# Kernel tuning notes

Hardware: AMD Instinct MI355X
Metric: run time of the kernel (lower is better)

The kernel has to match this reference:

```python
import jax, jax.numpy as jnp
import numpy as np

DIM = 512        # token feature dim
HID = 1024       # expert hidden dim (dim * 2)
E = 16           # num_experts
N = 8192         # num tokens
TOPK = 2         # experts active per token (routing sparsity)


def setup_inputs() -> dict:
    key = jax.random.key(0)
    k_x, k_s, k_w1, k_w2 = jax.random.split(key, 4)
    x = jax.random.normal(k_x, (N, DIM), dtype=jnp.float32)
    # sparse routing scores: top-2 experts per token get nonzero score, rest 0
    scores = jax.random.uniform(k_s, (N, E), dtype=jnp.float32)
    vals, idx = jax.lax.top_k(scores, TOPK)
    routing_tensor = jnp.zeros((N, E), jnp.float32).at[jnp.arange(N)[:, None], idx].set(vals)
    # per-expert MLP params (depth=2, bias=True): Linear(DIM->HID), GELU, Linear(HID->DIM)
    W1 = jax.random.normal(k_w1, (E, DIM, HID), dtype=jnp.float32) * (1.0 / np.sqrt(DIM))
    b1 = jnp.zeros((E, HID), jnp.float32)
    W2 = jax.random.normal(k_w2, (E, HID, DIM), dtype=jnp.float32) * (1.0 / np.sqrt(HID))
    b2 = jnp.zeros((E, DIM), jnp.float32)
    return {"x": x, "routing_tensor": routing_tensor, "W1": W1, "b1": b1, "W2": W2, "b2": b2}


def reference(x, routing_tensor, W1, b1, W2, b2):
    # out[n] = sum_e routing[n,e] * MLP_e(x[n]); rows with score 0 contribute 0,
    # which is exactly the original mask-gather / scatter-add semantics.
    h = jax.nn.gelu(jnp.einsum('nd,edh->enh', x, W1) + b1[:, None, :], approximate=False)
    y = jnp.einsum('enh,ehd->end', h, W2) + b2[:, None, :]  # [E, N, DIM]
    return jnp.einsum('end,ne->nd', y, routing_tensor)       # combine weighted by scores
```

## Files before the change

### kernel.cpp

```cpp
#include <hip/hip_runtime.h>
#include <hip/hip_bf16.h>

#define NTOK 8192
#define DIM 512
#define HID 1024
#define NE 16
#define CAP 1280
#define MT 20

typedef __attribute__((ext_vector_type(8))) short short8;
typedef __attribute__((ext_vector_type(8))) unsigned short us8;
typedef __attribute__((ext_vector_type(4))) float f32x4;

static __device__ __forceinline__ unsigned short f2bf(float f) {
    __hip_bfloat16 h = __float2bfloat16(f);
    return __builtin_bit_cast(unsigned short, h);
}

static __device__ __forceinline__ void gl_lds16(const unsigned short* g, unsigned short* l) {
    __builtin_amdgcn_global_load_lds(
        (const __attribute__((address_space(1))) unsigned int*)g,
        (__attribute__((address_space(3))) unsigned int*)l, 16, 0, 0);
}

static __device__ __forceinline__ float gelu_f(float v) {
    float u = v * (0.7978845608f + 0.0356774081f * v * v);
    return v / (1.0f + __expf(-2.0f * u));
}

__global__ __launch_bounds__(256) void route_fill(const float* __restrict__ routing,
                                                  int* __restrict__ cnt,
                                                  int* __restrict__ sidx,
                                                  float* __restrict__ wtb) {
    __shared__ int lcnt[NE], lbase[NE];
    int t = threadIdx.x;
    int n = blockIdx.x * 256 + t;
    if (t < NE) lcnt[t] = 0;
    __syncthreads();
    int mye[2]; float myw[2]; int mypos[2]; int slot = 0;
    #pragma unroll
    for (int e = 0; e < NE; e++) {
        float r = routing[n * NE + e];
        if (r != 0.0f && slot < 2) {
            mye[slot] = e; myw[slot] = r;
            mypos[slot] = atomicAdd(&lcnt[e], 1);
            slot++;
        }
    }
    __syncthreads();
    if (t < NE) lbase[t] = atomicAdd(&cnt[t], lcnt[t]);
    __syncthreads();
    for (int s = 0; s < slot; s++) {
        int e = mye[s];
        int p = lbase[e] + mypos[s];
        if (p < CAP) { sidx[e * CAP + p] = n * 2 + s; wtb[e * CAP + p] = myw[s]; }
    }
}

__global__ __launch_bounds__(256) void prep2(const float* __restrict__ W1,
                                             const float* __restrict__ W2,
                                             unsigned short* __restrict__ w1t,
                                             unsigned short* __restrict__ w2t,
                                             const float* __restrict__ x,
                                             const int* __restrict__ cnt,
                                             const int* __restrict__ sidx,
                                             unsigned short* __restrict__ xg) {
    int b = blockIdx.x;
    int t = threadIdx.x;
    if (b < 4096) {
        __shared__ float tile[64][65];
        const float* src; unsigned short* dst; int R, C, bx, by;
        if (b < 2048) {
            int e = b >> 7, rem = b & 127; bx = rem & 15; by = rem >> 4;
            R = DIM; C = HID;
            src = W1 + (size_t)e * R * C; dst = w1t + (size_t)e * R * C;
        } else {
            int bb = b - 2048;
            int e = bb >> 7, rem = bb & 127; bx = rem & 7; by = rem >> 3;
            R = HID; C = DIM;
            src = W2 + (size_t)e * R * C; dst = w2t + (size_t)e * R * C;
        }
        int c0 = bx * 64, r0 = by * 64;
        int tx = t & 15, ty = t >> 4;
        #pragma unroll
        for (int i = 0; i < 4; i++) {
            float4 v = *(const float4*)(src + (size_t)(r0 + ty + i * 16) * C + c0 + tx * 4);
            tile[ty + i * 16][tx * 4 + 0] = v.x;
            tile[ty + i * 16][tx * 4 + 1] = v.y;
            tile[ty + i * 16][tx * 4 + 2] = v.z;
            tile[ty + i * 16][tx * 4 + 3] = v.w;
        }
        __syncthreads();
        int seg = t & 7;
        #pragma unroll
        for (int i = 0; i < 2; i++) {
            int dr = (t >> 3) + i * 32;
            us8 o;
            #pragma unroll
            for (int j = 0; j < 8; j++)
                o[j] = f2bf(tile[seg * 8 + j][dr]);
            *(us8*)(dst + (size_t)(c0 + dr) * R + r0 + seg * 8) = o;
        }
    } else {
        int gi = b - 4096;
        int lane = t & 63, rl = t >> 6;
        int row = gi * 4 + rl;
        int e = row / CAP, r = row - e * CAP;
        int c = cnt[e]; c = c > CAP ? CAP : c;
        us8 o;
        if (r < c) {
            int n = sidx[row] >> 1;
            const float* xr = x + (size_t)n * DIM + lane * 8;
            float4 v0 = *(const float4*)xr;
            float4 v1 = *(const float4*)(xr + 4);
            o[0] = f2bf(v0.x); o[1] = f2bf(v0.y); o[2] = f2bf(v0.z); o[3] = f2bf(v0.w);
            o[4] = f2bf(v1.x); o[5] = f2bf(v1.y); o[6] = f2bf(v1.z); o[7] = f2bf(v1.w);
        } else {
            #pragma unroll
            for (int j = 0; j < 8; j++) o[j] = 0;
        }
        *(us8*)(xg + (size_t)row * DIM + lane * 8) = o;
    }
}

template <int K>
__device__ __forceinline__ void mfma_main64(const unsigned short* __restrict__ A,
                                            const unsigned short* __restrict__ B,
                                            unsigned short* As, unsigned short* Bs,
                                            f32x4 acc[2][4]) {
    int t = threadIdx.x;
    int wave = t >> 6, lane = t & 63;
    int wm = wave >> 1, wn = wave & 1;
    int quad = lane >> 4, l16 = lane & 15;
    int lr = lane >> 3;
    int col = (lane & 7) << 3;
    for (int kc = 0; kc < K; kc += 64) {
        __syncthreads();
        #pragma unroll
        for (int j = 0; j < 2; j++) {
            int rb = wave * 16 + j * 8;
            gl_lds16(A + (size_t)(rb + lr) * K + kc + col, As + rb * 64);
        }
        #pragma unroll
        for (int j = 0; j < 4; j++) {
            int rb = wave * 32 + j * 8;
            gl_lds16(B + (size_t)(rb + lr) * K + kc + col, Bs + rb * 64);
        }
        __syncthreads();
        #pragma unroll
        for (int kk = 0; kk < 64; kk += 32) {
            short8 av[2], bv[4];
            #pragma unroll
            for (int mt = 0; mt < 2; mt++)
                av[mt] = *(const short8*)(&As[(wm * 32 + mt * 16 + l16) * 64 + kk + quad * 8]);
            #pragma unroll
            for (int nt = 0; nt < 4; nt++)
                bv[nt] = *(const short8*)(&Bs[(wn * 64 + nt * 16 + l16) * 64 + kk + quad * 8]);
            #pragma unroll
            for (int mt = 0; mt < 2; mt++)
                #pragma unroll
                for (int nt = 0; nt < 4; nt++)
                    acc[mt][nt] = __builtin_amdgcn_mfma_f32_16x16x32_bf16(
                        av[mt], bv[nt], acc[mt][nt], 0, 0, 0);
        }
    }
}


__global__ __launch_bounds__(256, 5) void gemm1_gelu(
    const unsigned short* __restrict__ xg, const unsigned short* __restrict__ w1t,
    const float* __restrict__ b1, const int* __restrict__ cnt,
    unsigned short* __restrict__ hbuf) {
    __shared__ __align__(16) unsigned short As[64 * 64];
    __shared__ __align__(16) unsigned short Bs[128 * 64];
    int L = blockIdx.x;
    int cc = L & 7, n = (L >> 3) & 7, g = L >> 6;
    int pi = cc + (g << 3);
    int e = pi / MT, m = pi % MT;
    int c = cnt[e]; c = c > CAP ? CAP : c;
    int m0 = m * 64;
    if (m0 >= c) return;
    int n0 = n * 128;
    const unsigned short* A = xg + ((size_t)e * CAP + m0) * DIM;
    const unsigned short* B = w1t + ((size_t)e * HID + n0) * DIM;
    f32x4 z = {0.f, 0.f, 0.f, 0.f};
    f32x4 acc[2][4];
    #pragma unroll
    for (int mt = 0; mt < 2; mt++)
        #pragma unroll
        for (int nt = 0; nt < 4; nt++) acc[mt][nt] = z;
    mfma_main64<DIM>(A, B, As, Bs, acc);
    int t = threadIdx.x;
    int wave = t >> 6, lane = t & 63;
    int wm = wave >> 1, wn = wave & 1, quad = lane >> 4, l16 = lane & 15;
    #pragma unroll
    for (int nt = 0; nt < 4; nt++) {
        int gn = n0 + wn * 64 + nt * 16 + l16;
        float bias = b1[e * HID + gn];
        #pragma unroll
        for (int mt = 0; mt < 2; mt++) {
            #pragma unroll
            for (int r = 0; r < 4; r++) {
                int gm = m0 + wm * 32 + mt * 16 + quad * 4 + r;
                float v = acc[mt][nt][r] + bias;
                hbuf[((size_t)e * CAP + gm) * HID + gn] = f2bf(gelu_f(v));
            }
        }
    }
}

__global__ __launch_bounds__(256, 5) void gemm2_store(
    const unsigned short* __restrict__ hbuf, const unsigned short* __restrict__ w2t,
    const float* __restrict__ b2, const int* __restrict__ cnt,
    const int* __restrict__ sidx, const float* __restrict__ wtb,
    float* __restrict__ ybuf) {
    __shared__ __align__(16) unsigned short As[64 * 64];
    __shared__ __align__(16) unsigned short Bs[128 * 64];
    int L = blockIdx.x;
    int cc = L & 7, n = (L >> 3) & 3, g = L >> 5;
    int pi = cc + (g << 3);
    int e = pi / MT, m = pi % MT;
    int c = cnt[e]; c = c > CAP ? CAP : c;
    int m0 = m * 64;
    if (m0 >= c) return;
    int n0 = n * 128;
    const unsigned short* A = hbuf + ((size_t)e * CAP + m0) * HID;
    const unsigned short* B = w2t + ((size_t)e * DIM + n0) * HID;
    f32x4 z = {0.f, 0.f, 0.f, 0.f};
    f32x4 acc[2][4];
    #pragma unroll
    for (int mt = 0; mt < 2; mt++)
        #pragma unroll
        for (int nt = 0; nt < 4; nt++) acc[mt][nt] = z;
    mfma_main64<HID>(A, B, As, Bs, acc);
    int t = threadIdx.x;
    int wave = t >> 6, lane = t & 63;
    int wm = wave >> 1, wn = wave & 1, quad = lane >> 4, l16 = lane & 15;
    #pragma unroll
    for (int mt = 0; mt < 2; mt++) {
        #pragma unroll
        for (int r = 0; r < 4; r++) {
            int gm = m0 + wm * 32 + mt * 16 + quad * 4 + r;
            if (gm < c) {
                int si = sidx[e * CAP + gm];
                float wgt = wtb[e * CAP + gm];
                float* yrow = ybuf + (size_t)si * DIM;
                #pragma unroll
                for (int nt = 0; nt < 4; nt++) {
                    int gn = n0 + wn * 64 + nt * 16 + l16;
                    yrow[gn] = wgt * (acc[mt][nt][r] + b2[e * DIM + gn]);
                }
            }
        }
    }
}

__global__ void combine(const float* __restrict__ yb, float* __restrict__ out) {
    int i = blockIdx.x * 256 + threadIdx.x;
    int n = i >> 7, d4 = i & 127;
    float4 a = ((const float4*)(yb + (size_t)(2 * n) * DIM))[d4];
    float4 b = ((const float4*)(yb + (size_t)(2 * n + 1) * DIM))[d4];
    float4 o;
    o.x = a.x + b.x; o.y = a.y + b.y; o.z = a.z + b.z; o.w = a.w + b.w;
    ((float4*)(out + (size_t)n * DIM))[d4] = o;
}

extern "C" void kernel_launch(void* const* d_in, const int* in_sizes, int n_in,
                              void* d_out, int out_size, void* d_ws, size_t ws_size,
                              hipStream_t stream) {
    const float* x       = (const float*)d_in[0];
    const float* routing = (const float*)d_in[1];
    const float* W1      = (const float*)d_in[2];
    const float* b1      = (const float*)d_in[3];
    const float* W2      = (const float*)d_in[4];
    const float* b2      = (const float*)d_in[5];
    float* out = (float*)d_out;

    char* w = (char*)d_ws;
    int*   cnt  = (int*)w;
    int*   sidx = (int*)(w + 256);
    float* wtb  = (float*)(w + 256 + NE * CAP * 4);
    char* base = w + 256 + NE * CAP * 8;
    unsigned short* xg  = (unsigned short*)base;
    unsigned short* hb  = xg + (size_t)NE * CAP * DIM;
    unsigned short* w1t = hb + (size_t)NE * CAP * HID;
    unsigned short* w2t = w1t + (size_t)NE * HID * DIM;
    float* ybuf = (float*)(w2t + (size_t)NE * DIM * HID);

    hipMemsetAsync(cnt, 0, 256, stream);

    route_fill<<<NTOK / 256, 256, 0, stream>>>(routing, cnt, sidx, wtb);
    prep2<<<4096 + 5120, 256, 0, stream>>>(W1, W2, w1t, w2t, x, cnt, sidx, xg);

    gemm1_gelu<<<8 * MT * NE, 256, 0, stream>>>(xg, w1t, b1, cnt, hb);
    gemm2_store<<<4 * MT * NE, 256, 0, stream>>>(hb, w2t, b2, cnt, sidx, wtb, ybuf);
    combine<<<(NTOK * DIM / 4) / 256, 256, 0, stream>>>(ybuf, out);
}
```

Before: 223.0 us.

## Store per-expert outputs in bf16 and hoist bias loads in gemm2

The intermediate per-(token,slot) output buffer changes from fp32 to bf16, which halves the scattered writes in gemm2 and the reads in the combine kernel. The combine kernel now processes 8 elements per thread, and gemm2 loads the b2 bias once per thread instead of inside the store loop. Launch bounds for both GEMMs rise from 5 to 6 waves per SIMD. In exchange, the output picks up extra bf16 rounding before the final fp32 sum, and the tighter launch bound may force register spills.

```diff
diff --git a/kernel.cpp b/kernel.cpp
--- a/kernel.cpp
+++ b/kernel.cpp
@@ -15,6 +15,10 @@
 static __device__ __forceinline__ unsigned short f2bf(float f) {
     __hip_bfloat16 h = __float2bfloat16(f);
     return __builtin_bit_cast(unsigned short, h);
+}
+static __device__ __forceinline__ float bf2f(unsigned short u) {
+    unsigned int v = (unsigned int)u << 16;
+    return __builtin_bit_cast(float, v);
 }
 
 static __device__ __forceinline__ void gl_lds16(const unsigned short* g, unsigned short* l) {
@@ -167,7 +171,7 @@
 }
 
 
-__global__ __launch_bounds__(256, 5) void gemm1_gelu(
+__global__ __launch_bounds__(256, 6) void gemm1_gelu(
     const unsigned short* __restrict__ xg, const unsigned short* __restrict__ w1t,
     const float* __restrict__ b1, const int* __restrict__ cnt,
     unsigned short* __restrict__ hbuf) {
@@ -209,11 +213,11 @@
     }
 }
 
-__global__ __launch_bounds__(256, 5) void gemm2_store(
+__global__ __launch_bounds__(256, 6) void gemm2_store(
     const unsigned short* __restrict__ hbuf, const unsigned short* __restrict__ w2t,
     const float* __restrict__ b2, const int* __restrict__ cnt,
     const int* __restrict__ sidx, const float* __restrict__ wtb,
-    float* __restrict__ ybuf) {
+    unsigned short* __restrict__ ybuf) {
     __shared__ __align__(16) unsigned short As[64 * 64];
     __shared__ __align__(16) unsigned short Bs[128 * 64];
     int L = blockIdx.x;
@@ -236,6 +240,10 @@
     int t = threadIdx.x;
     int wave = t >> 6, lane = t & 63;
     int wm = wave >> 1, wn = wave & 1, quad = lane >> 4, l16 = lane & 15;
+    float b2v[4];
+    #pragma unroll
+    for (int nt = 0; nt < 4; nt++)
+        b2v[nt] = b2[e * DIM + n0 + wn * 64 + nt * 16 + l16];
     #pragma unroll
     for (int mt = 0; mt < 2; mt++) {
         #pragma unroll
@@ -244,25 +252,30 @@
             if (gm < c) {
                 int si = sidx[e * CAP + gm];
                 float wgt = wtb[e * CAP + gm];
-                float* yrow = ybuf + (size_t)si * DIM;
+                unsigned short* yrow = ybuf + (size_t)si * DIM;
                 #pragma unroll
                 for (int nt = 0; nt < 4; nt++) {
                     int gn = n0 + wn * 64 + nt * 16 + l16;
-                    yrow[gn] = wgt * (acc[mt][nt][r] + b2[e * DIM + gn]);
+                    yrow[gn] = f2bf(wgt * (acc[mt][nt][r] + b2v[nt]));
                 }
             }
         }
     }
 }
 
-__global__ void combine(const float* __restrict__ yb, float* __restrict__ out) {
+__global__ void combine(const unsigned short* __restrict__ yb, float* __restrict__ out) {
     int i = blockIdx.x * 256 + threadIdx.x;
-    int n = i >> 7, d4 = i & 127;
-    float4 a = ((const float4*)(yb + (size_t)(2 * n) * DIM))[d4];
-    float4 b = ((const float4*)(yb + (size_t)(2 * n + 1) * DIM))[d4];
-    float4 o;
-    o.x = a.x + b.x; o.y = a.y + b.y; o.z = a.z + b.z; o.w = a.w + b.w;
-    ((float4*)(out + (size_t)n * DIM))[d4] = o;
+    int n = i >> 6, d8 = i & 63;
+    us8 a = ((const us8*)(yb + (size_t)(2 * n) * DIM))[d8];
+    us8 b = ((const us8*)(yb + (size_t)(2 * n + 1) * DIM))[d8];
+    float4 o0, o1;
+    o0.x = bf2f(a[0]) + bf2f(b[0]); o0.y = bf2f(a[1]) + bf2f(b[1]);
+    o0.z = bf2f(a[2]) + bf2f(b[2]); o0.w = bf2f(a[3]) + bf2f(b[3]);
+    o1.x = bf2f(a[4]) + bf2f(b[4]); o1.y = bf2f(a[5]) + bf2f(b[5]);
+    o1.z = bf2f(a[6]) + bf2f(b[6]); o1.w = bf2f(a[7]) + bf2f(b[7]);
+    float* op = out + (size_t)n * DIM + d8 * 8;
+    *(float4*)op = o0;
+    *(float4*)(op + 4) = o1;
 }
 
 extern "C" void kernel_launch(void* const* d_in, const int* in_sizes, int n_in,
@@ -285,7 +298,7 @@
     unsigned short* hb  = xg + (size_t)NE * CAP * DIM;
     unsigned short* w1t = hb + (size_t)NE * CAP * HID;
     unsigned short* w2t = w1t + (size_t)NE * HID * DIM;
-    float* ybuf = (float*)(w2t + (size_t)NE * DIM * HID);
+    unsigned short* ybuf = w2t + (size_t)NE * DIM * HID;
 
     hipMemsetAsync(cnt, 0, 256, stream);
 
@@ -294,5 +307,5 @@
 
     gemm1_gelu<<<8 * MT * NE, 256, 0, stream>>>(xg, w1t, b1, cnt, hb);
     gemm2_store<<<4 * MT * NE, 256, 0, stream>>>(hb, w2t, b2, cnt, sidx, wtb, ybuf);
-    combine<<<(NTOK * DIM / 4) / 256, 256, 0, stream>>>(ybuf, out);
-}
+    combine<<<(NTOK * DIM / 8) / 256, 256, 0, stream>>>(ybuf, out);
+}
```

Result: slower. 268.5 us (+20.4%).
